# Kernel optimization log

Measured on AMD Instinct MI355X. Metric: run time of the kernel, lower is better.

## Reference

```python
import jax, jax.numpy as jnp
import numpy as np


def _closest_dist_sum(p1, p2):
    # p1: [B, N, 3], p2: [B, M, 3]
    # Euclidean distance via the expanded quadratic form; matches
    # torch.norm(p1 - p2, 2, dim=3) -> min over p2 -> sum over all.
    d2 = (jnp.sum(p1 * p1, axis=-1)[:, :, None]
          + jnp.sum(p2 * p2, axis=-1)[:, None, :]
          - 2.0 * jnp.einsum('bnd,bmd->bnm', p1, p2))  # [B, N, M]
    d = jnp.sqrt(jnp.maximum(d2, 0.0))
    return jnp.sum(jnp.min(d, axis=2))


def setup_inputs() -> dict:
    key = jax.random.key(0)
    k1, k2 = jax.random.split(key)
    shape_xyz = jax.random.normal(k1, (8, 8192, 6), dtype=jnp.float32)
    skel_xyz = jax.random.normal(k2, (8, 2048, 3), dtype=jnp.float32)
    return {"shape_xyz": shape_xyz, "skel_xyz": skel_xyz}


def reference(shape_xyz, skel_xyz):
    # normals (shape_xyz[:, :, 3:6]) are extracted but unused in the loss
    pts = shape_xyz[:, :, :3]
    cd1 = _closest_dist_sum(pts, skel_xyz)   # shape -> skeleton
    cd2 = _closest_dist_sum(skel_xyz, pts)   # skeleton -> shape
    loss_cd = (cd1 + cd2) * 0.0001
    return loss_cd
```

## Files before the change

kernel.cpp:

```cpp
#include <hip/hip_runtime.h>

#define BATCH   8
#define SHAPE_N 8192
#define SKEL_M  2048
#define CHUNK   1024

typedef short bf16x8 __attribute__((ext_vector_type(8)));
typedef float f32x16 __attribute__((ext_vector_type(16)));
union FragU { bf16x8 v; uint4 u4; };

__device__ __forceinline__ unsigned int f2bf(float a) {
    unsigned int u = __float_as_uint(a);
    return (u + 0x7FFFu + ((u >> 16) & 1u)) >> 16;
}
__device__ __forceinline__ float bf2f(unsigned int h) {
    return __uint_as_float(h << 16);
}
__device__ __forceinline__ unsigned int pack2(unsigned int lo, unsigned int hi) {
    return lo | (hi << 16);
}
__device__ __forceinline__ void bfsplit(float v, unsigned int& h, unsigned int& l) {
    h = f2bf(v);
    l = f2bf(v - bf2f(h));
}

template <int SA, int SB>
__device__ __forceinline__ float cd_scan(
    const float* __restrict__ Araw,
    const float* __restrict__ Braw,
    uint4* sB, float* p_ra)
{
    const int tid = threadIdx.x;
    const int l = tid & 63;

    const float* p = Araw + (size_t)(l & 31) * SA;
    const float x = p[0], y = p[1], z = p[2];
    *p_ra = x * x + y * y + z * z;
    unsigned int hx, lx, hy, ly, hz, lz;
    bfsplit(x, hx, lx); bfsplit(y, hy, ly); bfsplit(z, hz, lz);
    const unsigned int one = 0x3F80u;
    FragU bf;
    if (l < 32) {
        bf.u4 = make_uint4(pack2(hx, hy), pack2(hz, one),
                           pack2(lx, ly), pack2(lz, one));
    } else {
        bf.u4 = make_uint4(pack2(hx, hy), pack2(hz, 0u), 0u, 0u);
    }

    const f32x16 Z = {0,0,0,0,0,0,0,0,0,0,0,0,0,0,0,0};
    f32x16 Dmin;
#pragma unroll
    for (int j = 0; j < 16; ++j) Dmin[j] = 3.4e38f;
    const unsigned int off0 = (unsigned int)((l >> 5) * 512 + (l & 31) * 16);

    for (int c = 0; c < 2048; c += CHUNK) {
        __syncthreads();
        const float* src = Braw + (size_t)c * SB;
        for (int i = tid; i < CHUNK; i += 256) {
            const float* q = src + (size_t)i * SB;
            const float bx = q[0], by = q[1], bz = q[2];
            const float cx = -2.f * bx, cy = -2.f * by, cz = -2.f * bz;
            const float rb = bx * bx + by * by + bz * bz;
            unsigned int chx, clx, chy, cly, chz, clz, rbh, rbl;
            bfsplit(cx, chx, clx); bfsplit(cy, chy, cly); bfsplit(cz, chz, clz);
            bfsplit(rb, rbh, rbl);
            const int g = i >> 5, r = i & 31;
            sB[g * 64 + r]      = make_uint4(pack2(chx, chy), pack2(chz, rbh),
                                             pack2(chx, chy), pack2(chz, rbl));
            sB[g * 64 + 32 + r] = make_uint4(pack2(clx, cly), pack2(clz, 0u),
                                             0u, 0u);
        }
        __syncthreads();

        unsigned int o = off0;
#pragma unroll 8
        for (int g = 0; g < CHUNK / 32; ++g) {
            FragU af;
            af.u4 = *(const uint4*)((const char*)sB + o);
            o += 1024;
            f32x16 D = __builtin_amdgcn_mfma_f32_32x32x16_bf16(af.v, bf.v, Z, 0, 0, 0);
#pragma unroll
            for (int j = 0; j < 16; ++j) Dmin[j] = fminf(Dmin[j], D[j]);
        }
    }
    const float m0 = fminf(fminf(Dmin[0],  Dmin[1]),  fminf(Dmin[2],  Dmin[3]));
    const float m1 = fminf(fminf(Dmin[4],  Dmin[5]),  fminf(Dmin[6],  Dmin[7]));
    const float m2 = fminf(fminf(Dmin[8],  Dmin[9]),  fminf(Dmin[10], Dmin[11]));
    const float m3 = fminf(fminf(Dmin[12], Dmin[13]), fminf(Dmin[14], Dmin[15]));
    float rmin = fminf(fminf(m0, m1), fminf(m2, m3));
    rmin = fminf(rmin, __shfl_xor(rmin, 32, 64));
    return rmin;
}

__global__ __launch_bounds__(256) void cd_main(
    const float* __restrict__ shape, const float* __restrict__ skel,
    unsigned int* __restrict__ ws, float* __restrict__ out)
{
    __shared__ uint4 sB[CHUNK * 2];
    __shared__ float s_wsum[4];
    const int tid = threadIdx.x;
    const int l = tid & 63, wv = tid >> 6;
    const int bid = blockIdx.x;

    if (bid < 512) {
        const int b = bid >> 6, sub = bid & 63;
        float ra;
        const float rmin = cd_scan<6, 3>(
            shape + ((size_t)b * SHAPE_N + sub * 128 + wv * 32) * 6,
            skel + (size_t)b * SKEL_M * 3, sB, &ra);
        float d = (l < 32) ? sqrtf(fmaxf(ra + rmin, 0.f)) : 0.f;
        for (int o = 32; o; o >>= 1) d += __shfl_down(d, o, 64);
        if (l == 0) s_wsum[wv] = d;
        __syncthreads();
        if (tid == 0)
            atomicAdd(out, (s_wsum[0] + s_wsum[1] + s_wsum[2] + s_wsum[3]) * 1e-4f);
    } else {
        const int j = bid - 512;
        const int b = j >> 6, rem = j & 63;
        const int asub = rem >> 2, bs = rem & 3;
        float ra;
        const float rmin = cd_scan<3, 6>(
            skel + ((size_t)b * SKEL_M + asub * 128 + wv * 32) * 3,
            shape + ((size_t)b * SHAPE_N + bs * 2048) * 6, sB, &ra);
        if (l < 32) {
            const float v = fmaxf(ra + rmin, 0.f);
            atomicMin(&ws[b * SKEL_M + asub * 128 + wv * 32 + l],
                      __float_as_uint(v));
        }
    }
}

__global__ __launch_bounds__(256) void cd_finalize(
    const uint4* __restrict__ ws, float* __restrict__ out)
{
    __shared__ float s_wsum[4];
    const uint4 v = ws[blockIdx.x * 256 + threadIdx.x];
    float s = sqrtf(__uint_as_float(v.x)) + sqrtf(__uint_as_float(v.y)) +
              sqrtf(__uint_as_float(v.z)) + sqrtf(__uint_as_float(v.w));
    for (int o = 32; o; o >>= 1) s += __shfl_down(s, o, 64);
    const int lane = threadIdx.x & 63, wave = threadIdx.x >> 6;
    if (lane == 0) s_wsum[wave] = s;
    __syncthreads();
    if (threadIdx.x == 0)
        atomicAdd(out, (s_wsum[0] + s_wsum[1] + s_wsum[2] + s_wsum[3]) * 1e-4f);
}

extern "C" void kernel_launch(void* const* d_in, const int* in_sizes, int n_in,
                              void* d_out, int out_size, void* d_ws, size_t ws_size,
                              hipStream_t stream) {
    const float* shape = (const float*)d_in[0];
    const float* skel  = (const float*)d_in[1];
    float* out         = (float*)d_out;
    unsigned int* ws   = (unsigned int*)d_ws;

    hipMemsetAsync(out, 0, sizeof(float), stream);
    hipMemsetAsync(ws, 0xFF, (size_t)BATCH * SKEL_M * sizeof(unsigned int), stream);
    cd_main<<<1024, 256, 0, stream>>>(shape, skel, ws, out);
    cd_finalize<<<BATCH * SKEL_M / 1024, 256, 0, stream>>>((const uint4*)ws, out);
}
```

Before: 80.21 us.

## Replace atomics and memsets with per-block partials and a single-block reduce

Per-block partial sums and per-split minimum values are now written to distinct workspace slots instead of using atomicAdd/atomicMin. A single 1024-thread block then takes the min across the four splits, applies sqrt and sums everything, which removes both memsets and the atomic traffic. The inner MFMA loop also reduces each 16-element tile to one scalar minimum per iteration rather than keeping 16 running minima, trading register pressure for more serial fmin work per step. The final reduce runs on one block, so it is serialized but small.

New measurement: 75.73 us (median of 2 runs). 5.6% less time.

```diff
diff --git a/kernel.cpp b/kernel.cpp
--- a/kernel.cpp
+++ b/kernel.cpp
@@ -4,6 +4,8 @@
 #define SHAPE_N 8192
 #define SKEL_M  2048
 #define CHUNK   1024
+
+#define WS2_OFF 512
 
 typedef short bf16x8 __attribute__((ext_vector_type(8)));
 typedef float f32x16 __attribute__((ext_vector_type(16)));
@@ -48,9 +50,7 @@
     }
 
     const f32x16 Z = {0,0,0,0,0,0,0,0,0,0,0,0,0,0,0,0};
-    f32x16 Dmin;
-#pragma unroll
-    for (int j = 0; j < 16; ++j) Dmin[j] = 3.4e38f;
+    float rmin = 3.4e38f;
     const unsigned int off0 = (unsigned int)((l >> 5) * 512 + (l & 31) * 16);
 
     for (int c = 0; c < 2048; c += CHUNK) {
@@ -79,22 +79,23 @@
             af.u4 = *(const uint4*)((const char*)sB + o);
             o += 1024;
             f32x16 D = __builtin_amdgcn_mfma_f32_32x32x16_bf16(af.v, bf.v, Z, 0, 0, 0);
-#pragma unroll
-            for (int j = 0; j < 16; ++j) Dmin[j] = fminf(Dmin[j], D[j]);
+            const float t0 = fminf(fminf(D[0],  D[1]),  D[2]);
+            const float t1 = fminf(fminf(D[3],  D[4]),  D[5]);
+            const float t2 = fminf(fminf(D[6],  D[7]),  D[8]);
+            const float t3 = fminf(fminf(D[9],  D[10]), D[11]);
+            const float t4 = fminf(fminf(D[12], D[13]), D[14]);
+            const float u0 = fminf(fminf(t0, t1), t2);
+            const float u1 = fminf(fminf(t3, t4), D[15]);
+            rmin = fminf(rmin, fminf(u0, u1));
         }
     }
-    const float m0 = fminf(fminf(Dmin[0],  Dmin[1]),  fminf(Dmin[2],  Dmin[3]));
-    const float m1 = fminf(fminf(Dmin[4],  Dmin[5]),  fminf(Dmin[6],  Dmin[7]));
-    const float m2 = fminf(fminf(Dmin[8],  Dmin[9]),  fminf(Dmin[10], Dmin[11]));
-    const float m3 = fminf(fminf(Dmin[12], Dmin[13]), fminf(Dmin[14], Dmin[15]));
-    float rmin = fminf(fminf(m0, m1), fminf(m2, m3));
     rmin = fminf(rmin, __shfl_xor(rmin, 32, 64));
     return rmin;
 }
 
 __global__ __launch_bounds__(256) void cd_main(
     const float* __restrict__ shape, const float* __restrict__ skel,
-    unsigned int* __restrict__ ws, float* __restrict__ out)
+    float* __restrict__ ws)
 {
     __shared__ uint4 sB[CHUNK * 2];
     __shared__ float s_wsum[4];
@@ -113,7 +114,7 @@
         if (l == 0) s_wsum[wv] = d;
         __syncthreads();
         if (tid == 0)
-            atomicAdd(out, (s_wsum[0] + s_wsum[1] + s_wsum[2] + s_wsum[3]) * 1e-4f);
+            ws[bid] = s_wsum[0] + s_wsum[1] + s_wsum[2] + s_wsum[3];
     } else {
         const int j = bid - 512;
         const int b = j >> 6, rem = j & 63;
@@ -122,27 +123,46 @@
         const float rmin = cd_scan<3, 6>(
             skel + ((size_t)b * SKEL_M + asub * 128 + wv * 32) * 3,
             shape + ((size_t)b * SHAPE_N + bs * 2048) * 6, sB, &ra);
-        if (l < 32) {
-            const float v = fmaxf(ra + rmin, 0.f);
-            atomicMin(&ws[b * SKEL_M + asub * 128 + wv * 32 + l],
-                      __float_as_uint(v));
-        }
+        if (l < 32)
+            ws[WS2_OFF + bs * (BATCH * SKEL_M) + b * SKEL_M +
+               asub * 128 + wv * 32 + l] = ra + rmin;
     }
 }
 
-__global__ __launch_bounds__(256) void cd_finalize(
-    const uint4* __restrict__ ws, float* __restrict__ out)
+__global__ __launch_bounds__(1024) void cd_reduce(
+    const float* __restrict__ ws, float* __restrict__ out)
 {
-    __shared__ float s_wsum[4];
-    const uint4 v = ws[blockIdx.x * 256 + threadIdx.x];
-    float s = sqrtf(__uint_as_float(v.x)) + sqrtf(__uint_as_float(v.y)) +
-              sqrtf(__uint_as_float(v.z)) + sqrtf(__uint_as_float(v.w));
+    __shared__ float s_wsum[16];
+    const int t = threadIdx.x;
+    float s = 0.f;
+
+    const float4* w4 = (const float4*)(ws + WS2_OFF);
+#pragma unroll
+    for (int r = 0; r < 4; ++r) {
+        const int i4 = r * 1024 + t;
+        float4 v0 = w4[i4];
+        const float4 v1 = w4[4096 + i4];
+        const float4 v2 = w4[8192 + i4];
+        const float4 v3 = w4[12288 + i4];
+        v0.x = fminf(fminf(v0.x, v1.x), fminf(v2.x, v3.x));
+        v0.y = fminf(fminf(v0.y, v1.y), fminf(v2.y, v3.y));
+        v0.z = fminf(fminf(v0.z, v1.z), fminf(v2.z, v3.z));
+        v0.w = fminf(fminf(v0.w, v1.w), fminf(v2.w, v3.w));
+        s += sqrtf(fmaxf(v0.x, 0.f)) + sqrtf(fmaxf(v0.y, 0.f)) +
+             sqrtf(fmaxf(v0.z, 0.f)) + sqrtf(fmaxf(v0.w, 0.f));
+    }
+    if (t < 512) s += ws[t];
+
     for (int o = 32; o; o >>= 1) s += __shfl_down(s, o, 64);
-    const int lane = threadIdx.x & 63, wave = threadIdx.x >> 6;
+    const int lane = t & 63, wave = t >> 6;
     if (lane == 0) s_wsum[wave] = s;
     __syncthreads();
-    if (threadIdx.x == 0)
-        atomicAdd(out, (s_wsum[0] + s_wsum[1] + s_wsum[2] + s_wsum[3]) * 1e-4f);
+    if (t == 0) {
+        float tot = 0.f;
+#pragma unroll
+        for (int w = 0; w < 16; ++w) tot += s_wsum[w];
+        out[0] = tot * 1e-4f;
+    }
 }
 
 extern "C" void kernel_launch(void* const* d_in, const int* in_sizes, int n_in,
@@ -151,10 +171,8 @@
     const float* shape = (const float*)d_in[0];
     const float* skel  = (const float*)d_in[1];
     float* out         = (float*)d_out;
-    unsigned int* ws   = (unsigned int*)d_ws;
+    float* ws          = (float*)d_ws;
 
-    hipMemsetAsync(out, 0, sizeof(float), stream);
-    hipMemsetAsync(ws, 0xFF, (size_t)BATCH * SKEL_M * sizeof(unsigned int), stream);
-    cd_main<<<1024, 256, 0, stream>>>(shape, skel, ws, out);
-    cd_finalize<<<BATCH * SKEL_M / 1024, 256, 0, stream>>>((const uint4*)ws, out);
+    cd_main<<<1024, 256, 0, stream>>>(shape, skel, ws);
+    cd_reduce<<<1, 1024, 0, stream>>>(ws, out);
 }
```
